# Kernel tuning notes

Measured on AMD Instinct MI355X. Metric: run time of the kernel, lower is better.

Reference implementation:

```python
import jax, jax.numpy as jnp
import numpy as np

DIM = 128
HEADS = 8
WIN = 4
B, D, H, W = 2, 48, 48, 48


def setup_inputs() -> dict:
    key = jax.random.key(0)
    k1, k2, k3 = jax.random.split(key, 3)
    x = jax.random.normal(k1, (B, DIM, D, H, W), dtype=jnp.float32)
    # torch.nn.Linear default init ~ U(-1/sqrt(fan_in), 1/sqrt(fan_in)); scaled normal is fine
    Wqkv = jax.random.normal(k2, (3 * DIM, DIM), dtype=jnp.float32) * (DIM ** -0.5)
    Wout = jax.random.normal(k3, (DIM, DIM), dtype=jnp.float32) * (DIM ** -0.5)
    bout = jnp.zeros((DIM,), dtype=jnp.float32)
    return {"x": x, "Wqkv": Wqkv, "Wout": Wout, "bout": bout}


def reference(x, Wqkv, Wout, bout):
    b, c, d, h, w = x.shape
    heads, win = HEADS, WIN
    hd = c // heads
    scale = c ** (-0.5)  # NOTE: original scales by dim**-0.5, not head_dim**-0.5
    nd, nh, nw = d // win, h // win, w // win

    xf = jnp.transpose(x, (0, 2, 3, 4, 1))          # (B,D,H,W,C)
    qkv = jnp.einsum('bdhwc,ec->bdhwe', xf, Wqkv)    # (B,D,H,W,3C)
    q, k, v = jnp.split(qkv, 3, axis=-1)

    def to_windows(t):
        # (B,D,H,W,C) -> (B,heads,num_windows,tokens,head_dim) matching unfold3d ordering
        t = t.reshape(b, nd, win, nh, win, nw, win, heads, hd)
        t = jnp.transpose(t, (0, 7, 1, 3, 5, 2, 4, 6, 8))  # B,hds,nd,nh,nw,wd,wh,ww,hd
        return t.reshape(b, heads, nd * nh * nw, win ** 3, hd)

    qw, kw, vw = to_windows(q), to_windows(k), to_windows(v)

    attn = jax.nn.softmax(jnp.einsum('bhntd,bhnsd->bhnts', qw, kw) * scale, axis=-1)
    out = jnp.einsum('bhnts,bhnsd->bhntd', attn, vw)  # (B,heads,N,T,hd)

    # Faithful to original: tokens stay in window order, then reinterpreted as spatial
    out = out.reshape(b, heads, -1, hd)
    out = jnp.transpose(out, (0, 2, 1, 3)).reshape(b, -1, heads * hd)
    out = out @ Wout.T + bout                         # (B, D*H*W, C)
    out = out.reshape(b, d, h, w, c)
    return jnp.transpose(out, (0, 4, 1, 2, 3))        # (B,C,D,H,W)
```

## Files before the change

kernel.cpp:

```cpp
#include <hip/hip_runtime.h>
#include <hip/hip_bf16.h>
#include <stdint.h>

#define NWIN 1728
#define SPD  110592

typedef __attribute__((ext_vector_type(8)))  short  short8;
typedef __attribute__((ext_vector_type(4)))  short  short4v;
typedef __attribute__((ext_vector_type(4)))  float  f32x4;
typedef __attribute__((ext_vector_type(16))) float  f32x16;

#define SRS 136
#define SQS 24
#define SVS 72

#define CFENCE() asm volatile("" ::: "memory")
#define LFENCE() asm volatile("s_waitcnt lgkmcnt(0)" ::: "memory")

__device__ __forceinline__ short f2bf(float f) {
  uint32_t u = __builtin_bit_cast(uint32_t, f);
  u += 0x7FFFu + ((u >> 16) & 1u);
  return (short)(u >> 16);
}

__global__ void cvt_weights_kernel(const float* __restrict__ wqkv,
                                   const float* __restrict__ wout,
                                   short* __restrict__ wq_bf,
                                   short* __restrict__ wo_bf) {
  int i = blockIdx.x * 256 + threadIdx.x;
  wq_bf[i] = f2bf(wqkv[i]);
  if (i < 128 * 128) wo_bf[i] = f2bf(wout[i]);
}

__global__ __launch_bounds__(256, 3)
void win_attn_kernel(const float* __restrict__ x,
                     const short* __restrict__ wqkv_bf,
                     const short* __restrict__ wout_bf,
                     const float* __restrict__ bout,
                     float* __restrict__ out) {
  __shared__ __align__(16) short sU[4 * 32 * SVS];
  __shared__ __align__(16) short sq[4][64 * SQS];
  __shared__ __align__(16) short sk[4][64 * SQS];
  __shared__ __align__(16) short sv[4][16 * SVS];

  const int tid  = threadIdx.x;
  const int lane = tid & 63;
  const int w    = tid >> 6;
  const int m16 = lane & 15, q16 = lane >> 4;
  const int m32 = lane & 31, h32 = lane >> 5;

  const int blk  = blockIdx.x;
  const int g    = (blk & 7) * 432 + (blk >> 3);
  const int b    = g / NWIN;
  const int win  = g - b * NWIN;
  const int id   = win / 144;
  const int ihw  = win - id * 144;
  const int ih   = ihw / 12;
  const int iw   = ihw - ih * 12;

  short* sR  = sU;
  short* spw = sU + w * (32 * SVS);

  short8 wpre[4];
  #pragma unroll
  for (int ks = 0; ks < 4; ++ks)
    wpre[ks] = *reinterpret_cast<const short8*>(
        wqkv_bf + ((2 * w) * 16 + m16) * 128 + ks * 32 + q16 * 8);

  const float* xb = x + (size_t)b * (128 * SPD) + id * (4 * 2304) + ih * (4 * 48) + iw * 4;
  uint32_t* sRw = reinterpret_cast<uint32_t*>(sR);
  #pragma unroll
  for (int i = 0; i < 4; ++i) {
    int row = i * 4 + w;
    int cp  = lane;
    const float* base = xb + (size_t)(cp * 2) * SPD + (row >> 2) * 2304 + (row & 3) * 48;
    float4 v0 = *reinterpret_cast<const float4*>(base);
    float4 v1 = *reinterpret_cast<const float4*>(base + SPD);
    int t = (row >> 2) * 16 + (row & 3) * 4;
    sRw[(t + 0) * (SRS / 2) + cp] = (uint32_t)(uint16_t)f2bf(v0.x) | ((uint32_t)(uint16_t)f2bf(v1.x) << 16);
    sRw[(t + 1) * (SRS / 2) + cp] = (uint32_t)(uint16_t)f2bf(v0.y) | ((uint32_t)(uint16_t)f2bf(v1.y) << 16);
    sRw[(t + 2) * (SRS / 2) + cp] = (uint32_t)(uint16_t)f2bf(v0.z) | ((uint32_t)(uint16_t)f2bf(v1.z) << 16);
    sRw[(t + 3) * (SRS / 2) + cp] = (uint32_t)(uint16_t)f2bf(v0.w) | ((uint32_t)(uint16_t)f2bf(v1.w) << 16);
  }
  __syncthreads();

  short8 afrag[4][4];
  #pragma unroll
  for (int mt = 0; mt < 4; ++mt)
    #pragma unroll
    for (int ks = 0; ks < 4; ++ks)
      afrag[mt][ks] = *reinterpret_cast<const short8*>(
          &sR[(mt * 16 + m16) * SRS + ks * 32 + q16 * 8]);
  __syncthreads();

  f32x4 oacc[2][4];
  f32x4 inv [2][4];
  #pragma unroll
  for (int i = 0; i < 2; ++i)
    #pragma unroll
    for (int j = 0; j < 4; ++j)
      #pragma unroll
      for (int r = 0; r < 4; ++r) oacc[i][j][r] = 0.0f;

  const float scale = 0.08838834764831845f;
  f32x16 z16;
  #pragma unroll
  for (int i = 0; i < 16; ++i) z16[i] = 0.0f;
  f32x4 z4;
  #pragma unroll
  for (int i = 0; i < 4; ++i) z4[i] = 0.0f;
  short8 ones8;
  #pragma unroll
  for (int i = 0; i < 8; ++i) ones8[i] = (short)0x3F80;

  #pragma unroll
  for (int hh = 0; hh < 2; ++hh) {
    const int h = 2 * w + hh;

    #pragma unroll
    for (int which = 0; which < 3; ++which) {
      const int et = which * 8 + h;
      short8 wb[4];
      #pragma unroll
      for (int ks = 0; ks < 4; ++ks)
        wb[ks] = (hh == 0 && which == 0) ? wpre[ks]
               : *reinterpret_cast<const short8*>(
                     wqkv_bf + (et * 16 + m16) * 128 + ks * 32 + q16 * 8);
      f32x4 acc[4];
      #pragma unroll
      for (int mt = 0; mt < 4; ++mt)
        #pragma unroll
        for (int r = 0; r < 4; ++r) acc[mt][r] = 0.0f;
      #pragma unroll
      for (int ks = 0; ks < 4; ++ks)
        #pragma unroll
        for (int mt = 0; mt < 4; ++mt)
          acc[mt] = __builtin_amdgcn_mfma_f32_16x16x32_bf16(afrag[mt][ks], wb[ks], acc[mt], 0, 0, 0);

      if (which == 0) {
        #pragma unroll
        for (int mt = 0; mt < 4; ++mt)
          #pragma unroll
          for (int r = 0; r < 4; ++r)
            sq[w][(mt * 16 + q16 * 4 + r) * SQS + m16] = f2bf(acc[mt][r]);
      } else if (which == 1) {
        #pragma unroll
        for (int mt = 0; mt < 4; ++mt)
          #pragma unroll
          for (int r = 0; r < 4; ++r)
            sk[w][(mt * 16 + q16 * 4 + r) * SQS + m16] = f2bf(acc[mt][r]);
      } else {
        #pragma unroll
        for (int mt = 0; mt < 4; ++mt) {
          short4v pk;
          pk[0] = f2bf(acc[mt][0]); pk[1] = f2bf(acc[mt][1]);
          pk[2] = f2bf(acc[mt][2]); pk[3] = f2bf(acc[mt][3]);
          *reinterpret_cast<short4v*>(&sv[w][m16 * SVS + mt * 16 + q16 * 4]) = pk;
        }
      }
    }
    LFENCE();

    short8 kf0 = *reinterpret_cast<const short8*>(&sk[w][(m32) * SQS + h32 * 8]);
    short8 kf1 = *reinterpret_cast<const short8*>(&sk[w][(32 + m32) * SQS + h32 * 8]);
    short8 vf0 = *reinterpret_cast<const short8*>(&sv[w][m16 * SVS + q16 * 8]);
    short8 vf1 = *reinterpret_cast<const short8*>(&sv[w][m16 * SVS + 32 + q16 * 8]);
    #pragma unroll
    for (int mt2 = 0; mt2 < 2; ++mt2) {
      short8 qf = *reinterpret_cast<const short8*>(&sq[w][(mt2 * 32 + m32) * SQS + h32 * 8]);
      f32x16 s0 = __builtin_amdgcn_mfma_f32_32x32x16_bf16(qf, kf0, z16, 0, 0, 0);
      f32x16 s1 = __builtin_amdgcn_mfma_f32_32x32x16_bf16(qf, kf1, z16, 0, 0, 0);
      CFENCE();
      #pragma unroll
      for (int r = 0; r < 16; ++r) {
        int row = (r & 3) + 8 * (r >> 2) + 4 * h32;
        spw[row * SVS + m32]      = f2bf(__expf(s0[r] * scale));
        spw[row * SVS + 32 + m32] = f2bf(__expf(s1[r] * scale));
      }
      LFENCE();
      #pragma unroll
      for (int sub = 0; sub < 2; ++sub) {
        short8 pf0 = *reinterpret_cast<const short8*>(&spw[(sub * 16 + m16) * SVS + q16 * 8]);
        short8 pf1 = *reinterpret_cast<const short8*>(&spw[(sub * 16 + m16) * SVS + 32 + q16 * 8]);
        int tile = mt2 * 2 + sub;
        oacc[hh][tile] = __builtin_amdgcn_mfma_f32_16x16x32_bf16(pf0, vf0, oacc[hh][tile], 0, 0, 0);
        oacc[hh][tile] = __builtin_amdgcn_mfma_f32_16x16x32_bf16(pf1, vf1, oacc[hh][tile], 0, 0, 0);
        f32x4 rs = __builtin_amdgcn_mfma_f32_16x16x32_bf16(pf0, ones8, z4, 0, 0, 0);
        rs       = __builtin_amdgcn_mfma_f32_16x16x32_bf16(pf1, ones8, rs, 0, 0, 0);
        #pragma unroll
        for (int r = 0; r < 4; ++r) inv[hh][tile][r] = __builtin_amdgcn_rcpf(rs[r]);
      }
    }
  }

  short8 wob[2][4];
  #pragma unroll
  for (int ntl = 0; ntl < 2; ++ntl)
    #pragma unroll
    for (int ks = 0; ks < 4; ++ks)
      wob[ntl][ks] = *reinterpret_cast<const short8*>(
          wout_bf + ((2 * w + ntl) * 16 + m16) * 128 + ks * 32 + q16 * 8);
  float bias0 = bout[(2 * w) * 16 + m16];
  float bias1 = bout[(2 * w + 1) * 16 + m16];

  __syncthreads();

  #pragma unroll
  for (int hh = 0; hh < 2; ++hh) {
    int c0 = (2 * w + hh) * 16;
    #pragma unroll
    for (int mt = 0; mt < 4; ++mt)
      #pragma unroll
      for (int r = 0; r < 4; ++r)
        sR[(mt * 16 + q16 * 4 + r) * SRS + c0 + m16] = f2bf(oacc[hh][mt][r] * inv[hh][mt][r]);
  }
  __syncthreads();

  f32x4 outacc[4][2];
  #pragma unroll
  for (int i = 0; i < 4; ++i)
    #pragma unroll
    for (int j = 0; j < 2; ++j)
      #pragma unroll
      for (int r = 0; r < 4; ++r) outacc[i][j][r] = 0.0f;
  #pragma unroll
  for (int ks = 0; ks < 4; ++ks) {
    short8 af[4];
    #pragma unroll
    for (int mt = 0; mt < 4; ++mt)
      af[mt] = *reinterpret_cast<const short8*>(&sR[(mt * 16 + m16) * SRS + ks * 32 + q16 * 8]);
    #pragma unroll
    for (int ntl = 0; ntl < 2; ++ntl)
      #pragma unroll
      for (int mt = 0; mt < 4; ++mt)
        outacc[mt][ntl] = __builtin_amdgcn_mfma_f32_16x16x32_bf16(af[mt], wob[ntl][ks], outacc[mt][ntl], 0, 0, 0);
  }
  #pragma unroll
  for (int ntl = 0; ntl < 2; ++ntl) {
    int co = (2 * w + ntl) * 16 + m16;
    float bias = ntl ? bias1 : bias0;
    float* obase = out + (size_t)(b * 128 + co) * SPD + win * 64;
    #pragma unroll
    for (int mt = 0; mt < 4; ++mt) {
      float4 vres;
      vres.x = outacc[mt][ntl][0] + bias;
      vres.y = outacc[mt][ntl][1] + bias;
      vres.z = outacc[mt][ntl][2] + bias;
      vres.w = outacc[mt][ntl][3] + bias;
      *reinterpret_cast<float4*>(obase + mt * 16 + q16 * 4) = vres;
    }
  }
}

extern "C" void kernel_launch(void* const* d_in, const int* in_sizes, int n_in,
                              void* d_out, int out_size, void* d_ws, size_t ws_size,
                              hipStream_t stream) {
  const float* x    = (const float*)d_in[0];
  const float* wqkv = (const float*)d_in[1];
  const float* wout = (const float*)d_in[2];
  const float* bout = (const float*)d_in[3];
  short* wq_bf = (short*)d_ws;
  short* wo_bf = (short*)((char*)d_ws + 98304);
  cvt_weights_kernel<<<192, 256, 0, stream>>>(wqkv, wout, wq_bf, wo_bf);
  win_attn_kernel<<<2 * NWIN, 256, 0, stream>>>(x, wq_bf, wo_bf, bout, (float*)d_out);
}
```

Measured before the change: 278.3 us.

## Pool LDS per wave, write full 64x64 P tile, raise occupancy to 4

Replaces the separate q/k/v/P shared buffers with one per-wave pool of 4608 shorts. The full 64x64 probability tile now overwrites the q/k/v region, and all four P·V tiles are computed after a single LDS wait instead of two waits. Launch bounds rise from 3 to 4 blocks per SM, betting that the smaller LDS footprint allows more resident blocks. The risks are register spilling under the tighter bound and hazards from P overwriting q/k while other lanes may still be reading them.

```diff
diff --git a/kernel.cpp b/kernel.cpp
--- a/kernel.cpp
+++ b/kernel.cpp
@@ -13,6 +13,8 @@
 #define SRS 136
 #define SQS 24
 #define SVS 72
+
+#define PWS 4608
 
 #define CFENCE() asm volatile("" ::: "memory")
 #define LFENCE() asm volatile("s_waitcnt lgkmcnt(0)" ::: "memory")
@@ -32,16 +34,13 @@
   if (i < 128 * 128) wo_bf[i] = f2bf(wout[i]);
 }
 
-__global__ __launch_bounds__(256, 3)
+__global__ __launch_bounds__(256, 4)
 void win_attn_kernel(const float* __restrict__ x,
                      const short* __restrict__ wqkv_bf,
                      const short* __restrict__ wout_bf,
                      const float* __restrict__ bout,
                      float* __restrict__ out) {
-  __shared__ __align__(16) short sU[4 * 32 * SVS];
-  __shared__ __align__(16) short sq[4][64 * SQS];
-  __shared__ __align__(16) short sk[4][64 * SQS];
-  __shared__ __align__(16) short sv[4][16 * SVS];
+  __shared__ __align__(16) short pool[4 * PWS];
 
   const int tid  = threadIdx.x;
   const int lane = tid & 63;
@@ -58,8 +57,11 @@
   const int ih   = ihw / 12;
   const int iw   = ihw - ih * 12;
 
-  short* sR  = sU;
-  short* spw = sU + w * (32 * SVS);
+  short* const sR  = pool;
+  short* const sqw = pool + w * PWS;
+  short* const skw = sqw + 1536;
+  short* const svw = sqw + 3072;
+  short* const pw  = sqw;
 
   short8 wpre[4];
   #pragma unroll
@@ -142,55 +144,58 @@
         for (int mt = 0; mt < 4; ++mt)
           #pragma unroll
           for (int r = 0; r < 4; ++r)
-            sq[w][(mt * 16 + q16 * 4 + r) * SQS + m16] = f2bf(acc[mt][r]);
+            sqw[(mt * 16 + q16 * 4 + r) * SQS + m16] = f2bf(acc[mt][r]);
       } else if (which == 1) {
         #pragma unroll
         for (int mt = 0; mt < 4; ++mt)
           #pragma unroll
           for (int r = 0; r < 4; ++r)
-            sk[w][(mt * 16 + q16 * 4 + r) * SQS + m16] = f2bf(acc[mt][r]);
+            skw[(mt * 16 + q16 * 4 + r) * SQS + m16] = f2bf(acc[mt][r]);
       } else {
         #pragma unroll
         for (int mt = 0; mt < 4; ++mt) {
           short4v pk;
           pk[0] = f2bf(acc[mt][0]); pk[1] = f2bf(acc[mt][1]);
           pk[2] = f2bf(acc[mt][2]); pk[3] = f2bf(acc[mt][3]);
-          *reinterpret_cast<short4v*>(&sv[w][m16 * SVS + mt * 16 + q16 * 4]) = pk;
+          *reinterpret_cast<short4v*>(&svw[m16 * SVS + mt * 16 + q16 * 4]) = pk;
         }
       }
     }
     LFENCE();
 
-    short8 kf0 = *reinterpret_cast<const short8*>(&sk[w][(m32) * SQS + h32 * 8]);
-    short8 kf1 = *reinterpret_cast<const short8*>(&sk[w][(32 + m32) * SQS + h32 * 8]);
-    short8 vf0 = *reinterpret_cast<const short8*>(&sv[w][m16 * SVS + q16 * 8]);
-    short8 vf1 = *reinterpret_cast<const short8*>(&sv[w][m16 * SVS + 32 + q16 * 8]);
-    #pragma unroll
-    for (int mt2 = 0; mt2 < 2; ++mt2) {
-      short8 qf = *reinterpret_cast<const short8*>(&sq[w][(mt2 * 32 + m32) * SQS + h32 * 8]);
+    short8 kf0 = *reinterpret_cast<const short8*>(&skw[(m32) * SQS + h32 * 8]);
+    short8 kf1 = *reinterpret_cast<const short8*>(&skw[(32 + m32) * SQS + h32 * 8]);
+    short8 vf0 = *reinterpret_cast<const short8*>(&svw[m16 * SVS + q16 * 8]);
+    short8 vf1 = *reinterpret_cast<const short8*>(&svw[m16 * SVS + 32 + q16 * 8]);
+    short8 qfA = *reinterpret_cast<const short8*>(&sqw[(m32) * SQS + h32 * 8]);
+    short8 qfB = *reinterpret_cast<const short8*>(&sqw[(32 + m32) * SQS + h32 * 8]);
+
+    #pragma unroll
+    for (int c = 0; c < 2; ++c) {
+      short8 qf = c ? qfB : qfA;
       f32x16 s0 = __builtin_amdgcn_mfma_f32_32x32x16_bf16(qf, kf0, z16, 0, 0, 0);
       f32x16 s1 = __builtin_amdgcn_mfma_f32_32x32x16_bf16(qf, kf1, z16, 0, 0, 0);
       CFENCE();
       #pragma unroll
       for (int r = 0; r < 16; ++r) {
-        int row = (r & 3) + 8 * (r >> 2) + 4 * h32;
-        spw[row * SVS + m32]      = f2bf(__expf(s0[r] * scale));
-        spw[row * SVS + 32 + m32] = f2bf(__expf(s1[r] * scale));
+        int row = (r & 3) + 8 * (r >> 2) + 4 * h32 + 32 * c;
+        pw[row * SVS + m32]      = f2bf(__expf(s0[r] * scale));
+        pw[row * SVS + 32 + m32] = f2bf(__expf(s1[r] * scale));
       }
-      LFENCE();
-      #pragma unroll
-      for (int sub = 0; sub < 2; ++sub) {
-        short8 pf0 = *reinterpret_cast<const short8*>(&spw[(sub * 16 + m16) * SVS + q16 * 8]);
-        short8 pf1 = *reinterpret_cast<const short8*>(&spw[(sub * 16 + m16) * SVS + 32 + q16 * 8]);
-        int tile = mt2 * 2 + sub;
-        oacc[hh][tile] = __builtin_amdgcn_mfma_f32_16x16x32_bf16(pf0, vf0, oacc[hh][tile], 0, 0, 0);
-        oacc[hh][tile] = __builtin_amdgcn_mfma_f32_16x16x32_bf16(pf1, vf1, oacc[hh][tile], 0, 0, 0);
-        f32x4 rs = __builtin_amdgcn_mfma_f32_16x16x32_bf16(pf0, ones8, z4, 0, 0, 0);
-        rs       = __builtin_amdgcn_mfma_f32_16x16x32_bf16(pf1, ones8, rs, 0, 0, 0);
-        #pragma unroll
-        for (int r = 0; r < 4; ++r) inv[hh][tile][r] = __builtin_amdgcn_rcpf(rs[r]);
-      }
-    }
+    }
+    LFENCE();
+    #pragma unroll
+    for (int t = 0; t < 4; ++t) {
+      short8 pf0 = *reinterpret_cast<const short8*>(&pw[(t * 16 + m16) * SVS + q16 * 8]);
+      short8 pf1 = *reinterpret_cast<const short8*>(&pw[(t * 16 + m16) * SVS + 32 + q16 * 8]);
+      oacc[hh][t] = __builtin_amdgcn_mfma_f32_16x16x32_bf16(pf0, vf0, oacc[hh][t], 0, 0, 0);
+      oacc[hh][t] = __builtin_amdgcn_mfma_f32_16x16x32_bf16(pf1, vf1, oacc[hh][t], 0, 0, 0);
+      f32x4 rs = __builtin_amdgcn_mfma_f32_16x16x32_bf16(pf0, ones8, z4, 0, 0, 0);
+      rs       = __builtin_amdgcn_mfma_f32_16x16x32_bf16(pf1, ones8, rs, 0, 0, 0);
+      #pragma unroll
+      for (int r = 0; r < 4; ++r) inv[hh][t][r] = __builtin_amdgcn_rcpf(rs[r]);
+    }
+    CFENCE();
   }
 
   short8 wob[2][4];
```

Result: slower. 324.5 us (+16.6%).
